# Kernel tuning notes

Measured on AMD Instinct MI355X. Metric: run time of the kernel, lower is better.

The kernel has to match this reference:

```python
import jax, jax.numpy as jnp
import numpy as np

NUM_HEADS = 16
FIELD_SIZE = 512
SIGMA = 3.0
EMB = 1024


def _causal_kernel_fft(G, sigma):
    # kernel[i] = exp(-|i - G//2| / sigma) for i < G//2, else 0; normalized
    i = np.arange(G)
    dist = np.abs(i - G // 2)
    kernel = np.where(i >= G // 2, 0.0, np.exp(-dist / sigma)).astype(np.float32)
    kernel = kernel / (kernel.sum() + 1e-8)
    return jnp.asarray(np.fft.rfft(kernel), dtype=jnp.complex64)


def setup_inputs() -> dict:
    key = jax.random.key(0)
    ks = jax.random.split(key, 9)
    B, N, D = 4, 4096, EMB
    s = 1.0 / np.sqrt(D)
    return {
        "x": jax.random.normal(ks[0], (B, N, D), dtype=jnp.float32),
        "q_w": jax.random.uniform(ks[1], (D, D), minval=-s, maxval=s, dtype=jnp.float32),
        "q_b": jnp.zeros((D,), jnp.float32),
        "k_w": jax.random.uniform(ks[2], (D, D), minval=-s, maxval=s, dtype=jnp.float32),
        "k_b": jnp.zeros((D,), jnp.float32),
        "v_w": jax.random.uniform(ks[3], (D, D), minval=-s, maxval=s, dtype=jnp.float32),
        "v_b": jnp.zeros((D,), jnp.float32),
        "out_w": jax.random.uniform(ks[4], (D, D), minval=-s, maxval=s, dtype=jnp.float32),
        "out_b": jnp.zeros((D,), jnp.float32),
    }


def reference(x, q_w, q_b, k_w, k_b, v_w, v_b, out_w, out_b):
    B, N, D = x.shape
    H, hd, G = NUM_HEADS, D // NUM_HEADS, FIELD_SIZE

    # projections (q is computed in the original but unused downstream)
    q = x @ q_w.T + q_b  # noqa: F841 (faithful to original)
    k = (x @ k_w.T + k_b).reshape(B, N, H, hd).transpose(0, 2, 1, 3)  # (B,H,N,hd)
    v = (x @ v_w.T + v_b).reshape(B, N, H, hd).transpose(0, 2, 1, 3)

    # map sequence positions -> field bins (same for all b, h)
    pos = jnp.arange(N, dtype=jnp.float32) / max(N - 1, 1) * (G - 1)
    field_idx = jnp.clip(pos.astype(jnp.int32), 0, G - 1)  # (N,)

    # weighted values by key magnitude
    k_mag = jnp.linalg.norm(k, axis=-1, keepdims=True)  # (B,H,N,1)
    wv = v * k_mag  # (B,H,N,hd)

    # scatter-add tokens into field bins (vectorized over B,H,hd)
    field = jax.ops.segment_sum(wv.transpose(2, 0, 1, 3), field_idx,
                                num_segments=G)  # (G,B,H,hd)
    field = field.transpose(1, 2, 0, 3)  # (B,H,G,hd)

    # causal convolution along the field via FFT (circular, as in original)
    kfft = _causal_kernel_fft(G, SIGMA)
    f_fft = jnp.fft.rfft(field, n=G, axis=2)
    conv = jnp.fft.irfft(f_fft * kfft[None, None, :, None], n=G, axis=2)

    # gather back to token positions
    out = conv[:, :, field_idx, :]  # (B,H,N,hd)
    out = out.transpose(0, 2, 1, 3).reshape(B, N, D)
    return out @ out_w.T + out_b
```

## Files before the change

### kernel.cpp

```cpp
#include <hip/hip_runtime.h>
#include <hip/hip_bf16.h>

#define NPOS 4096
#define DIM  1024
#define GSZ  512

#define GAS __attribute__((address_space(1)))
#define LAS __attribute__((address_space(3)))

typedef __attribute__((ext_vector_type(8))) short bf16x8;
typedef __attribute__((ext_vector_type(4))) float f32x4;

__device__ __forceinline__ void async_load16(const void* g, void* l) {
  __builtin_amdgcn_global_load_lds((const GAS void*)g, (LAS void*)l, 16, 0, 0);
}

__device__ __forceinline__ int fidx_of(int n) {
  return (int)(((float)n / 4095.0f) * 511.0f);
}

__device__ __forceinline__ float bf2f(unsigned short s) {
  union { unsigned u; float f; } v; v.u = ((unsigned)s) << 16; return v.f;
}

__device__ __forceinline__ void bin_range(int g, int& i0, int& i1) {
  i0 = (g * 4095 + 510) / 511;
  while (i0 > 0 && fidx_of(i0 - 1) >= g) --i0;
  while (i0 < NPOS && fidx_of(i0) < g) ++i0;
  if (g == GSZ - 1) { i1 = NPOS; return; }
  i1 = ((g + 1) * 4095 + 510) / 511;
  while (i1 > 0 && fidx_of(i1 - 1) >= g + 1) --i1;
  while (i1 < NPOS && fidx_of(i1) < g + 1) ++i1;
}

__global__ __launch_bounds__(256) void cast_all(
    const float* __restrict__ x, const float* __restrict__ kw,
    const float* __restrict__ vw, const float* __restrict__ ow,
    __hip_bfloat16* __restrict__ xb, __hip_bfloat16* __restrict__ kvwb,
    __hip_bfloat16* __restrict__ outwb) {
  int blk = blockIdx.x;
  const float* src; __hip_bfloat16* dst; int off;
  if (blk < 16384)      { src = x;  dst = xb;              off = blk; }
  else if (blk < 17408) { src = kw; dst = kvwb;            off = blk - 16384; }
  else if (blk < 18432) { src = vw; dst = kvwb + 1048576;  off = blk - 17408; }
  else                  { src = ow; dst = outwb;           off = blk - 18432; }
  int i = (off * 256 + threadIdx.x) * 4;
  float4 f = *(const float4*)(src + i);
  ushort4 o;
  __hip_bfloat16 t;
  t = __float2bfloat16(f.x); o.x = *(unsigned short*)&t;
  t = __float2bfloat16(f.y); o.y = *(unsigned short*)&t;
  t = __float2bfloat16(f.z); o.z = *(unsigned short*)&t;
  t = __float2bfloat16(f.w); o.w = *(unsigned short*)&t;
  *(ushort4*)(dst + i) = o;
}


#define BAR()   __builtin_amdgcn_s_barrier()
#define LGKM0() do { asm volatile("s_waitcnt lgkmcnt(0)" ::: "memory"); \
                     __builtin_amdgcn_sched_barrier(0); } while (0)
#define VMW(N)  asm volatile("s_waitcnt vmcnt(" #N ")" ::: "memory")

#define STAGE_A(BUF, KT, C) \
  async_load16(ag0 + (size_t)(KT) * 64 + (size_t)(C) * 65536, &As[BUF][(C) * 4096 + ldst])
#define STAGE_B(BUF, KT, C) \
  async_load16(bg0 + (size_t)(KT) * 64 + (size_t)(C) * 65536, &Bs[BUF][(C) * 4096 + ldst])

#define STAGE_FULL(BUF, KT) do { \
    _Pragma("unroll") \
    for (int c_ = 0; c_ < 4; ++c_) { \
      STAGE_A(BUF, KT, c_); \
      STAGE_B(BUF, KT, c_); \
    } \
  } while (0)

#define LDA(BUF, MT, CB) (*(const bf16x8*)&As[BUF][abase + (MT) * 1024 + (CB)])
#define LDB(BUF, NT, CB) (*(const bf16x8*)&Bs[BUF][bbase + (NT) * 1024 + (CB)])

#define MFMA_Q(MQ, NQ, BF) do { \
    __builtin_amdgcn_s_setprio(1); \
    _Pragma("unroll") \
    for (int m_ = 0; m_ < 4; ++m_) { \
      _Pragma("unroll") \
      for (int n_ = 0; n_ < 2; ++n_) { \
        acc[(MQ)*4+m_][(NQ)*2+n_] = __builtin_amdgcn_mfma_f32_16x16x32_bf16( \
            af[m_][0], BF[n_][0], acc[(MQ)*4+m_][(NQ)*2+n_], 0, 0, 0); \
        acc[(MQ)*4+m_][(NQ)*2+n_] = __builtin_amdgcn_mfma_f32_16x16x32_bf16( \
            af[m_][1], BF[n_][1], acc[(MQ)*4+m_][(NQ)*2+n_], 0, 0, 0); \
      } \
    } \
    __builtin_amdgcn_s_setprio(0); \
  } while (0)

#define DO_TILE(BUF, KT) do { \
    const bool pf_ = (KT) + 2 < 16; \
     \
    _Pragma("unroll") \
    for (int m_ = 0; m_ < 4; ++m_) { af[m_][0] = LDA(BUF, m_, cb0); af[m_][1] = LDA(BUF, m_, cb1); } \
    _Pragma("unroll") \
    for (int n_ = 0; n_ < 2; ++n_) { b0f[n_][0] = LDB(BUF, n_, cb0); b0f[n_][1] = LDB(BUF, n_, cb1); } \
    BAR(); LGKM0(); \
    MFMA_Q(0, 0, b0f); \
    BAR(); \
     \
    _Pragma("unroll") \
    for (int n_ = 0; n_ < 2; ++n_) { b1f[n_][0] = LDB(BUF, 2 + n_, cb0); b1f[n_][1] = LDB(BUF, 2 + n_, cb1); } \
    if (pf_) { STAGE_A(BUF, (KT) + 2, 0); STAGE_A(BUF, (KT) + 2, 2); } \
    BAR(); LGKM0(); \
    MFMA_Q(0, 1, b1f); \
    BAR(); \
     \
    _Pragma("unroll") \
    for (int m_ = 0; m_ < 4; ++m_) { af[m_][0] = LDA(BUF, 4 + m_, cb0); af[m_][1] = LDA(BUF, 4 + m_, cb1); } \
    if (pf_) { STAGE_B(BUF, (KT) + 2, 0); STAGE_B(BUF, (KT) + 2, 1); \
               STAGE_B(BUF, (KT) + 2, 2); STAGE_B(BUF, (KT) + 2, 3); } \
    BAR(); LGKM0(); \
    MFMA_Q(1, 1, b1f); \
    BAR(); \
     \
    if (pf_) { STAGE_A(BUF, (KT) + 2, 1); STAGE_A(BUF, (KT) + 2, 3); } \
    MFMA_Q(1, 0, b0f); \
    if (pf_) { VMW(8); } else if ((KT) == 14) { VMW(0); } \
    BAR(); \
  } while (0)

__global__ __launch_bounds__(512, 2) void gemm_kv(
    const __hip_bfloat16* __restrict__ A,
    const __hip_bfloat16* __restrict__ B,
    const float* __restrict__ k_b, const float* __restrict__ v_b,
    __hip_bfloat16* __restrict__ Vb, float* __restrict__ knorm) {
  __shared__ __align__(16) __hip_bfloat16 As[2][16384];
  __shared__ __align__(16) __hip_bfloat16 Bs[2][16384];
  const int tid = threadIdx.x;

  const int l  = blockIdx.y * 64 + blockIdx.x;
  const int vv = (l & 7) * 64 + (l >> 3);
  const int bx = vv & 63, by = vv >> 6;
  const int bm = bx * 256;

  const int sb  = ((((tid & 7) * 16) ^ (((tid >> 3) & 7) << 4)) >> 1);
  const int r0  = tid >> 3;
  const __hip_bfloat16* ag0 = A + (size_t)(bm + r0) * 1024 + sb;
  const __hip_bfloat16* bg0 = B + (size_t)(by * 256 + r0) * 1024 + sb;
  const int ldst = tid * 8;

  const int wave = tid >> 6, lane = tid & 63;
  const int wr = wave >> 2, wc = wave & 3;
  const int m16 = lane & 15, quad = lane >> 4;
  const int swz  = (m16 & 7) << 4;
  const int cb0  = ((quad * 16)      ^ swz) >> 1;
  const int cb1  = ((quad * 16 + 64) ^ swz) >> 1;
  const int abase = wr * 8192 + m16 * 64;
  const int bbase = wc * 4096 + m16 * 64;

  f32x4 acc[8][4];
#pragma unroll
  for (int i = 0; i < 8; i++)
#pragma unroll
    for (int j = 0; j < 4; j++) acc[i][j] = (f32x4)0.f;

  bf16x8 af[4][2], b0f[2][2], b1f[2][2];

  STAGE_FULL(0, 0);
  STAGE_FULL(1, 1);
  VMW(8);
  BAR();

  for (int kt = 0; kt < 16; kt += 2) {
    DO_TILE(0, kt);
    DO_TILE(1, kt + 1);
  }

  if (by < 4) {
    const int head = by * 4 + wc;
    float bv[4];
#pragma unroll
    for (int nt = 0; nt < 4; nt++) bv[nt] = k_b[by * 256 + wc * 64 + nt * 16 + m16];
#pragma unroll
    for (int mt = 0; mt < 8; mt++) {
#pragma unroll
      for (int r = 0; r < 4; r++) {
        float s = 0.f;
#pragma unroll
        for (int nt = 0; nt < 4; nt++) {
          float t = acc[mt][nt][r] + bv[nt];
          s += t * t;
        }
        s += __shfl_xor(s, 1);
        s += __shfl_xor(s, 2);
        s += __shfl_xor(s, 4);
        s += __shfl_xor(s, 8);
        if (m16 == 0) {
          int row = bm + wr * 128 + mt * 16 + quad * 4 + r;
          knorm[(size_t)row * 16 + head] = sqrtf(s);
        }
      }
    }
  } else {
    const int colb = (by - 4) * 256 + wc * 64;
#pragma unroll
    for (int mt = 0; mt < 8; mt++) {
#pragma unroll
      for (int nt = 0; nt < 4; nt++) {
        int col = colb + nt * 16 + m16;
        float bvv = v_b[col];
#pragma unroll
        for (int r = 0; r < 4; r++) {
          int row = bm + wr * 128 + mt * 16 + quad * 4 + r;
          Vb[(size_t)row * 1024 + col] = __float2bfloat16(acc[mt][nt][r] + bvv);
        }
      }
    }
  }
}

__global__ __launch_bounds__(256) void gemm_outc(
    const __hip_bfloat16* __restrict__ A,
    const __hip_bfloat16* __restrict__ B,
    const float* __restrict__ bias,
    float* __restrict__ C) {
  const int K = 1024;
  __shared__ __align__(16) __hip_bfloat16 Aso[64 * 32];
  __shared__ __align__(16) __hip_bfloat16 Bso[64 * 32];
  const int tid = threadIdx.x;
  const int bm = blockIdx.x * 64, bn = blockIdx.y * 64;

  const int srow = tid >> 2;
  const int scol = (tid & 3) * 8;
  const __hip_bfloat16* ap = A + (size_t)(bm + srow) * K + scol;
  const __hip_bfloat16* bp = B + (size_t)(bn + srow) * K + scol;
  __hip_bfloat16* as = &Aso[srow * 32 + scol];
  __hip_bfloat16* bs = &Bso[srow * 32 + scol];

  const int wave = tid >> 6, lane = tid & 63;
  const int wm = (wave >> 1) * 32, wn = (wave & 1) * 32;
  const int m16 = lane & 15, quad = lane >> 4;

  f32x4 acc[2][2];
#pragma unroll
  for (int i = 0; i < 2; i++)
#pragma unroll
    for (int j = 0; j < 2; j++) acc[i][j] = (f32x4)0.f;

  for (int k0 = 0; k0 < K; k0 += 32) {
    async_load16(ap + k0, as);
    async_load16(bp + k0, bs);
    __syncthreads();
    bf16x8 afr[2], bfr[2];
#pragma unroll
    for (int mt = 0; mt < 2; mt++)
      afr[mt] = *(const bf16x8*)&Aso[(wm + mt * 16 + m16) * 32 + quad * 8];
#pragma unroll
    for (int nt = 0; nt < 2; nt++)
      bfr[nt] = *(const bf16x8*)&Bso[(wn + nt * 16 + m16) * 32 + quad * 8];
#pragma unroll
    for (int mt = 0; mt < 2; mt++)
#pragma unroll
      for (int nt = 0; nt < 2; nt++)
        acc[mt][nt] = __builtin_amdgcn_mfma_f32_16x16x32_bf16(afr[mt], bfr[nt], acc[mt][nt], 0, 0, 0);
    __syncthreads();
  }

#pragma unroll
  for (int mt = 0; mt < 2; mt++) {
#pragma unroll
    for (int r = 0; r < 4; r++) {
      int row = bm + wm + mt * 16 + quad * 4 + r;
      int bb = row >> 9, g = row & (GSZ - 1);
      int i0, i1;
      bin_range(g, i0, i1);
      float* obase = C + ((size_t)bb << 12) * DIM;
#pragma unroll
      for (int nt = 0; nt < 2; nt++) {
        int col = bn + wn + nt * 16 + m16;
        float val = acc[mt][nt][r] + bias[col];
        for (int n = i0; n < i1; ++n)
          obase[(size_t)n * DIM + col] = val;
      }
    }
  }
}

__global__ __launch_bounds__(256) void wv_field_kernel(
    const __hip_bfloat16* __restrict__ V, const float* __restrict__ knorm,
    float* __restrict__ field) {
  const int b = blockIdx.x, g = blockIdx.y;
  int i0, i1;
  bin_range(g, i0, i1);
  int cnt = i1 - i0;
  if (cnt > 9) cnt = 9;
  __shared__ float km[9][16];
  const int tid = threadIdx.x;
  if (tid < 144) {
    int r = tid >> 4, h = tid & 15;
    km[r][h] = (r < cnt) ? knorm[(size_t)(b * NPOS + i0 + r) * 16 + h] : 0.f;
  }
  __syncthreads();
  const int c0 = tid * 4, h = tid >> 4;
  const unsigned short* vbase = (const unsigned short*)V + (size_t)(b * NPOS + i0) * 1024 + c0;
  ushort4 vv[8];
  float ww[8];
#pragma unroll
  for (int j = 0; j < 8; ++j) {
    int jc = (j < cnt) ? j : 0;
    vv[j] = *(const ushort4*)(vbase + (size_t)jc * 1024);
    ww[j] = (j < cnt) ? km[j][h] : 0.f;
  }
  float a0 = 0.f, a1 = 0.f, a2 = 0.f, a3 = 0.f;
#pragma unroll
  for (int j = 0; j < 8; ++j) {
    a0 += ww[j] * bf2f(vv[j].x); a1 += ww[j] * bf2f(vv[j].y);
    a2 += ww[j] * bf2f(vv[j].z); a3 += ww[j] * bf2f(vv[j].w);
  }
  if (cnt == 9) {
    ushort4 v8 = *(const ushort4*)(vbase + (size_t)8 * 1024);
    float w8 = km[8][h];
    a0 += w8 * bf2f(v8.x); a1 += w8 * bf2f(v8.y);
    a2 += w8 * bf2f(v8.z); a3 += w8 * bf2f(v8.w);
  }
  *(float4*)(field + ((size_t)(b * GSZ + g)) * DIM + c0) = make_float4(a0, a1, a2, a3);
}

__global__ __launch_bounds__(256) void conv_ema_kernel(
    const float* __restrict__ field, __hip_bfloat16* __restrict__ convb) {
  const int b = blockIdx.x, h = blockIdx.y, n0 = blockIdx.z * 64;
  __shared__ float slab[128 * 64];
  const int tid = threadIdx.x;
  const float* fb = field + (size_t)b * GSZ * DIM + h * 64;
  for (int i = tid; i < 128 * 16; i += 256) {
    int row = i >> 4, c4 = i & 15;
    int gg = (n0 + 257 + row) & (GSZ - 1);
    *(float4*)&slab[row * 64 + c4 * 4] = *(const float4*)(fb + (size_t)gg * DIM + c4 * 4);
  }
  __syncthreads();
  const float a = 0.71653131057378927f;
  const float w1 = 1.0f - a;
  const int c = tid & 63, sub = tid >> 6;
  const int e0 = sub * 16;
  float acc = 0.f;
#pragma unroll 4
  for (int t = e0 + 79; t >= e0 + 16; --t)
    acc = w1 * slab[t * 64 + c] + a * acc;
#pragma unroll
  for (int t = e0 + 15; t >= e0; --t) {
    acc = w1 * slab[t * 64 + c] + a * acc;
    convb[((size_t)(b * GSZ) + n0 + t) * DIM + h * 64 + c] = __float2bfloat16(acc);
  }
}

extern "C" void kernel_launch(void* const* d_in, const int* in_sizes, int n_in,
                              void* d_out, int out_size, void* d_ws, size_t ws_size,
                              hipStream_t stream) {
  (void)in_sizes; (void)n_in; (void)out_size; (void)ws_size;
  const float* x     = (const float*)d_in[0];
  const float* k_w   = (const float*)d_in[3];
  const float* k_b   = (const float*)d_in[4];
  const float* v_w   = (const float*)d_in[5];
  const float* v_b   = (const float*)d_in[6];
  const float* out_w = (const float*)d_in[7];
  const float* out_b = (const float*)d_in[8];

  char* p = (char*)d_ws;
  __hip_bfloat16* xb    = (__hip_bfloat16*)p;         p += (size_t)16384 * 1024 * 2;
  __hip_bfloat16* kvwb  = (__hip_bfloat16*)p; p += (size_t)2048 * 1024 * 2;
  __hip_bfloat16* outwb = (__hip_bfloat16*)p; p += (size_t)1024 * 1024 * 2;
  __hip_bfloat16* Vb    = (__hip_bfloat16*)p; p += (size_t)16384 * 1024 * 2;
  float*          knorm = (float*)p;          p += (size_t)16384 * 16 * 4;
  float*          field = (float*)p;          p += (size_t)4 * 512 * 1024 * 4;
  __hip_bfloat16* convb = (__hip_bfloat16*)p;

  cast_all<<<19456, 256, 0, stream>>>(x, k_w, v_w, out_w, xb, kvwb, outwb);

  gemm_kv<<<dim3(64, 8), 512, 0, stream>>>(xb, kvwb, k_b, v_b, Vb, knorm);

  wv_field_kernel<<<dim3(4, 512), 256, 0, stream>>>(Vb, knorm, field);
  conv_ema_kernel<<<dim3(4, 16, 8), 256, 0, stream>>>(field, convb);

  gemm_outc<<<dim3(32, 16), 256, 0, stream>>>(convb, outwb, out_b, (float*)d_out);
}
```

Before: 261.5 us.

## Coalesce output scatter via LDS tile, widen cast loads, remap gemm_kv blocks

The output GEMM epilogue now stages its 64x64 result tile in shared memory and writes the expanded token rows with coalesced float4 stores, instead of each lane looping over scalar stores per row. The cast kernel handles 8 elements per thread with half the blocks. The gemm_kv block-to-tile mapping is changed so that each XCD works on a contiguous group of M tiles, which is meant to improve L2 reuse. The cost is extra LDS and a barrier in the epilogue.

```diff
diff --git a/kernel.cpp b/kernel.cpp
--- a/kernel.cpp
+++ b/kernel.cpp
@@ -23,14 +23,17 @@
   union { unsigned u; float f; } v; v.u = ((unsigned)s) << 16; return v.f;
 }
 
-__device__ __forceinline__ void bin_range(int g, int& i0, int& i1) {
-  i0 = (g * 4095 + 510) / 511;
+__device__ __forceinline__ int bin_start(int g) {
+  if (g >= GSZ) return NPOS;
+  int i0 = (g * 4095 + 510) / 511;
   while (i0 > 0 && fidx_of(i0 - 1) >= g) --i0;
   while (i0 < NPOS && fidx_of(i0) < g) ++i0;
-  if (g == GSZ - 1) { i1 = NPOS; return; }
-  i1 = ((g + 1) * 4095 + 510) / 511;
-  while (i1 > 0 && fidx_of(i1 - 1) >= g + 1) --i1;
-  while (i1 < NPOS && fidx_of(i1) < g + 1) ++i1;
+  return i0;
+}
+
+__device__ __forceinline__ void bin_range(int g, int& i0, int& i1) {
+  i0 = bin_start(g);
+  i1 = bin_start(g + 1);
 }
 
 __global__ __launch_bounds__(256) void cast_all(
@@ -40,19 +43,25 @@
     __hip_bfloat16* __restrict__ outwb) {
   int blk = blockIdx.x;
   const float* src; __hip_bfloat16* dst; int off;
-  if (blk < 16384)      { src = x;  dst = xb;              off = blk; }
-  else if (blk < 17408) { src = kw; dst = kvwb;            off = blk - 16384; }
-  else if (blk < 18432) { src = vw; dst = kvwb + 1048576;  off = blk - 17408; }
-  else                  { src = ow; dst = outwb;           off = blk - 18432; }
-  int i = (off * 256 + threadIdx.x) * 4;
-  float4 f = *(const float4*)(src + i);
-  ushort4 o;
+  if (blk < 8192)      { src = x;  dst = xb;              off = blk; }
+  else if (blk < 8704) { src = kw; dst = kvwb;            off = blk - 8192; }
+  else if (blk < 9216) { src = vw; dst = kvwb + 1048576;  off = blk - 8704; }
+  else                 { src = ow; dst = outwb;           off = blk - 9216; }
+  int i = (off * 256 + threadIdx.x) * 8;
+  float4 f0 = *(const float4*)(src + i);
+  float4 f1 = *(const float4*)(src + i + 4);
+  ushort4 o0, o1;
   __hip_bfloat16 t;
-  t = __float2bfloat16(f.x); o.x = *(unsigned short*)&t;
-  t = __float2bfloat16(f.y); o.y = *(unsigned short*)&t;
-  t = __float2bfloat16(f.z); o.z = *(unsigned short*)&t;
-  t = __float2bfloat16(f.w); o.w = *(unsigned short*)&t;
-  *(ushort4*)(dst + i) = o;
+  t = __float2bfloat16(f0.x); o0.x = *(unsigned short*)&t;
+  t = __float2bfloat16(f0.y); o0.y = *(unsigned short*)&t;
+  t = __float2bfloat16(f0.z); o0.z = *(unsigned short*)&t;
+  t = __float2bfloat16(f0.w); o0.w = *(unsigned short*)&t;
+  t = __float2bfloat16(f1.x); o1.x = *(unsigned short*)&t;
+  t = __float2bfloat16(f1.y); o1.y = *(unsigned short*)&t;
+  t = __float2bfloat16(f1.z); o1.z = *(unsigned short*)&t;
+  t = __float2bfloat16(f1.w); o1.w = *(unsigned short*)&t;
+  *(ushort4*)(dst + i) = o0;
+  *(ushort4*)(dst + i + 4) = o1;
 }
 
 
@@ -133,10 +142,10 @@
   __shared__ __align__(16) __hip_bfloat16 Bs[2][16384];
   const int tid = threadIdx.x;
 
-  const int l  = blockIdx.y * 64 + blockIdx.x;
-  const int vv = (l & 7) * 64 + (l >> 3);
-  const int bx = vv & 63, by = vv >> 6;
-  const int bm = bx * 256;
+  const int l   = blockIdx.y * 64 + blockIdx.x;
+  const int xcd = l & 7, j = l >> 3;
+  const int bx  = xcd * 8 + (j & 7), by = j >> 3;
+  const int bm  = bx * 256;
 
   const int sb  = ((((tid & 7) * 16) ^ (((tid >> 3) & 7) << 4)) >> 1);
   const int r0  = tid >> 3;
@@ -157,7 +166,7 @@
 #pragma unroll
   for (int i = 0; i < 8; i++)
 #pragma unroll
-    for (int j = 0; j < 4; j++) acc[i][j] = (f32x4)0.f;
+    for (int j2 = 0; j2 < 4; j2++) acc[i][j2] = (f32x4)0.f;
 
   bf16x8 af[4][2], b0f[2][2], b1f[2][2];
 
@@ -222,6 +231,7 @@
   const int K = 1024;
   __shared__ __align__(16) __hip_bfloat16 Aso[64 * 32];
   __shared__ __align__(16) __hip_bfloat16 Bso[64 * 32];
+  __shared__ __align__(16) float ctile[64 * 68];
   const int tid = threadIdx.x;
   const int bm = blockIdx.x * 64, bn = blockIdx.y * 64;
 
@@ -264,20 +274,30 @@
 #pragma unroll
   for (int mt = 0; mt < 2; mt++) {
 #pragma unroll
-    for (int r = 0; r < 4; r++) {
-      int row = bm + wm + mt * 16 + quad * 4 + r;
-      int bb = row >> 9, g = row & (GSZ - 1);
-      int i0, i1;
-      bin_range(g, i0, i1);
-      float* obase = C + ((size_t)bb << 12) * DIM;
-#pragma unroll
-      for (int nt = 0; nt < 2; nt++) {
-        int col = bn + wn + nt * 16 + m16;
-        float val = acc[mt][nt][r] + bias[col];
-        for (int n = i0; n < i1; ++n)
-          obase[(size_t)n * DIM + col] = val;
+    for (int nt = 0; nt < 2; nt++) {
+      int lcol = wn + nt * 16 + m16;
+      float bv = bias[bn + lcol];
+#pragma unroll
+      for (int r = 0; r < 4; r++) {
+        int lrow = wm + mt * 16 + quad * 4 + r;
+        ctile[lrow * 68 + lcol] = acc[mt][nt][r] + bv;
       }
     }
+  }
+  __syncthreads();
+
+  const int b  = bm >> 9;
+  const int g0 = bm & (GSZ - 1);
+  const int n0 = bin_start(g0);
+  const int n1 = bin_start(g0 + 64);
+  const int total = (n1 - n0) * 16;
+  float* obase = C + (((size_t)b << 12)) * DIM + bn;
+  for (int idx = tid; idx < total; idx += 256) {
+    int n  = n0 + (idx >> 4);
+    int c4 = (idx & 15) * 4;
+    int lg = fidx_of(n) - g0;
+    float4 v = *(const float4*)&ctile[lg * 68 + c4];
+    *(float4*)(obase + (size_t)n * DIM + c4) = v;
   }
 }
 
@@ -369,7 +389,7 @@
   float*          field = (float*)p;          p += (size_t)4 * 512 * 1024 * 4;
   __hip_bfloat16* convb = (__hip_bfloat16*)p;
 
-  cast_all<<<19456, 256, 0, stream>>>(x, k_w, v_w, out_w, xb, kvwb, outwb);
+  cast_all<<<9728, 256, 0, stream>>>(x, k_w, v_w, out_w, xb, kvwb, outwb);
 
   gemm_kv<<<dim3(64, 8), 512, 0, stream>>>(xb, kvwb, k_b, v_b, Vb, knorm);
 
```

After: 243.7 us. 1.07x faster.
